# Optimization experiments

Measured on AMD Instinct MI355X. Metric: run time of the kernel, lower is better.

Reference implementation:

```python
import jax, jax.numpy as jnp
import numpy as np

N, C, B, NPG, M, E = 131072, 128, 64, 2048, 64, 1048576
LN_EPS = 1e-5


def setup_inputs() -> dict:
    key = jax.random.key(0)
    ks = jax.random.split(key, 8)
    h = jax.random.normal(ks[0], (N, C), dtype=jnp.float32)
    edge_index = jax.random.randint(ks[1], (2, E), 0, N, dtype=jnp.int32)
    U = jax.random.normal(ks[2], (B, NPG, M), dtype=jnp.float32)
    W = jax.random.normal(ks[3], (M, C, C), dtype=jnp.float32) * 0.02
    lin_w = jax.random.normal(ks[4], (C, C), dtype=jnp.float32) * (1.0 / np.sqrt(C))
    lin_b = jax.random.normal(ks[5], (C,), dtype=jnp.float32) * 0.01
    ln_g = jnp.ones((C,), dtype=jnp.float32)
    ln_beta = jnp.zeros((C,), dtype=jnp.float32)
    return {"h": h, "U": U, "W": W, "lin_w": lin_w, "lin_b": lin_b,
            "ln_g": ln_g, "ln_beta": ln_beta, "edge_index": edge_index}


def _gfno_block(h, U, W, lin_w, lin_b, ln_g, ln_beta, edge_index):
    n_nodes, c = h.shape
    b, npg, m_avail = U.shape
    m = min(m_avail, W.shape[0])
    Um = U[:, :, :m]                      # [B, n, m]
    Wm = W[:m]                            # [m, C, C]
    # Block-diagonal spectral conv (equal-sized graphs -> batched einsum)
    hb = h.reshape(b, npg, c)             # [B, n, C]
    h_hat = jnp.einsum('bnm,bnc->bmc', Um, hb)        # U^T h per graph
    out_hat = jnp.einsum('bmc,mco->bmo', h_hat, Wm)   # per-mode mixing
    spec = jnp.einsum('bnm,bmo->bno', Um, out_hat).reshape(n_nodes, c)
    # Local scatter-mean aggregation
    src, dst = edge_index[0], edge_index[1]
    agg = jax.ops.segment_sum(h[src], dst, num_segments=n_nodes)   # [N, C]
    deg = jax.ops.segment_sum(jnp.ones((src.shape[0],), h.dtype), dst,
                              num_segments=n_nodes)
    deg = jnp.maximum(deg, 1.0)[:, None]
    local = (agg / deg) @ lin_w.T + lin_b
    # Residual + LayerNorm + GELU (exact, erf-based as torch default)
    x = h + spec + local
    mu = jnp.mean(x, axis=-1, keepdims=True)
    var = jnp.mean(jnp.square(x - mu), axis=-1, keepdims=True)
    xn = (x - mu) * jax.lax.rsqrt(var + LN_EPS) * ln_g + ln_beta
    return jax.nn.gelu(xn, approximate=False)


def reference(h, U, W, lin_w, lin_b, ln_g, ln_beta, edge_index):
    return _gfno_block(h, U, W, lin_w, lin_b, ln_g, ln_beta, edge_index)
```

## Files before the change

### kernel.cpp

```cpp
#include <hip/hip_runtime.h>
#include <math.h>

#define NN   131072
#define CN   128
#define BN   64
#define NPGN 2048
#define MN   64
#define EN   1048576

typedef unsigned short u16;
typedef unsigned int   u32;
typedef __attribute__((ext_vector_type(8))) short short8;
typedef __attribute__((ext_vector_type(4))) float f32x4;

__device__ __forceinline__ float bf2f(u16 u){ return __uint_as_float(((u32)u)<<16); }
__device__ __forceinline__ u16 f2bf(float f){
  u32 x = __float_as_uint(f);
  return (u16)((x + 0x7fffu + ((x>>16)&1u)) >> 16);
}

__global__ void k_count(const int* __restrict__ dst, int* __restrict__ deg){
  int e = blockIdx.x*256 + threadIdx.x;
  atomicAdd(&deg[dst[e]], 1);
}

__global__ void k_scan1(const int* __restrict__ deg, int* __restrict__ rowst, int* __restrict__ bsum){
  __shared__ int s[512];
  const int t = threadIdx.x;
  const int i = blockIdx.x*512 + t;
  int v = deg[i];
  s[t] = v;
  __syncthreads();
  for (int off=1; off<512; off<<=1){
    int a = (t>=off) ? s[t-off] : 0;
    __syncthreads();
    s[t] += a;
    __syncthreads();
  }
  rowst[i] = s[t] - v;
  if (t==511) bsum[blockIdx.x] = s[511];
}

__global__ void k_scan2(const int* __restrict__ bsum, int* __restrict__ bofs){
  __shared__ int s[256];
  const int t = threadIdx.x;
  int v = bsum[t];
  s[t] = v;
  __syncthreads();
  for (int off=1; off<256; off<<=1){
    int a = (t>=off) ? s[t-off] : 0;
    __syncthreads();
    s[t] += a;
    __syncthreads();
  }
  bofs[t] = s[t] - v;
}

__global__ void k_scan3(int* __restrict__ rowst, const int* __restrict__ bofs){
  int i = blockIdx.x*256 + threadIdx.x;
  rowst[i] += bofs[i>>9];
}

__global__ void k_fill(const int* __restrict__ src, const int* __restrict__ dst,
                       const int* __restrict__ rowst, int* __restrict__ cursor,
                       int* __restrict__ csr){
  int e = blockIdx.x*256 + threadIdx.x;
  int d = dst[e];
  int p = atomicAdd(&cursor[d], 1);
  csr[rowst[d] + p] = src[e];
}

__global__ void k_prepw(const float* __restrict__ lin_w, u16* __restrict__ wsw){
  int tid = blockIdx.x*256 + threadIdx.x;
  int g = tid >> 6, L = tid & 63;
  int ct = g >> 2, ks = g & 3;
  int o = L & 15, q = L >> 4;
  const float* srcp = lin_w + (ct*16+o)*CN + ks*32 + q*8;
  u16 tmp[8];
  #pragma unroll
  for (int j=0;j<8;++j) tmp[j] = f2bf(srcp[j]);
  *(uint4*)(wsw + (size_t)tid*8) = *(const uint4*)tmp;
}

__global__ void k_prep_h(const float* __restrict__ h, u16* __restrict__ h16, u16* __restrict__ ht16){
  __shared__ u16 st[CN*72];
  const int t = threadIdx.x;
  const int b = blockIdx.x >> 5;
  const int n0 = (blockIdx.x & 31)*64;
  const float* srcb = h + ((size_t)b*NPGN + n0)*CN;
  u16* natb = h16 + ((size_t)b*NPGN + n0)*CN;
  #pragma unroll
  for (int j=0;j<8;++j){
    int fidx = (j*256+t)*4;
    int r = fidx>>7, c = fidx&127;
    float4 v = *(const float4*)(srcb + fidx);
    u16 q0=f2bf(v.x), q1=f2bf(v.y), q2=f2bf(v.z), q3=f2bf(v.w);
    ushort4 nv; nv.x=q0; nv.y=q1; nv.z=q2; nv.w=q3;
    *(ushort4*)(natb + fidx) = nv;
    st[(c+0)*72 + r] = q0; st[(c+1)*72 + r] = q1;
    st[(c+2)*72 + r] = q2; st[(c+3)*72 + r] = q3;
  }
  __syncthreads();
  #pragma unroll
  for (int j=0;j<4;++j){
    int oidx = (j*256+t)*8;
    int c = oidx>>6, nn = oidx&63;
    uint4 v = *(const uint4*)&st[c*72 + nn];
    *(uint4*)(ht16 + ((size_t)b*CN + c)*NPGN + n0 + nn) = v;
  }
}

__global__ void k_prep_U(const float* __restrict__ U, u16* __restrict__ U16, u16* __restrict__ Ut16){
  __shared__ u16 st2[MN*136];
  const int t = threadIdx.x;
  const int b = blockIdx.x >> 4;
  const int n0 = (blockIdx.x & 15)*128;
  const float* srcb = U + ((size_t)b*NPGN + n0)*MN;
  u16* natb = U16 + ((size_t)b*NPGN + n0)*MN;
  #pragma unroll
  for (int j=0;j<8;++j){
    int fidx = (j*256+t)*4;
    int r = fidx>>6, mm = fidx&63;
    float4 v = *(const float4*)(srcb + fidx);
    u16 q0=f2bf(v.x), q1=f2bf(v.y), q2=f2bf(v.z), q3=f2bf(v.w);
    ushort4 nv; nv.x=q0; nv.y=q1; nv.z=q2; nv.w=q3;
    *(ushort4*)(natb + fidx) = nv;
    st2[(mm+0)*136 + r] = q0; st2[(mm+1)*136 + r] = q1;
    st2[(mm+2)*136 + r] = q2; st2[(mm+3)*136 + r] = q3;
  }
  __syncthreads();
  #pragma unroll
  for (int j=0;j<4;++j){
    int oidx = (j*256+t)*8;
    int mm = oidx>>7, nn = oidx&127;
    uint4 v = *(const uint4*)&st2[mm*136 + nn];
    *(uint4*)(Ut16 + ((size_t)b*MN + mm)*NPGN + n0 + nn) = v;
  }
}

__global__ __launch_bounds__(256) void k_hhat(const u16* __restrict__ Ut16,
                                              const u16* __restrict__ ht16,
                                              float* __restrict__ hp){
  const int t = threadIdx.x;
  const int L = t & 63, w = t >> 6;
  const int b = blockIdx.x >> 3, q = blockIdx.x & 7;
  const int lo = L & 15, qd = (L >> 4) << 3;
  f32x4 acc[8] = {};
  const u16* Arow  = Ut16 + ((size_t)(b*MN + w*16 + lo))*NPGN + q*256 + qd;
  const u16* Bbase = ht16 + ((size_t)(b*CN + lo))*NPGN + q*256 + qd;
  #pragma unroll
  for (int ks=0; ks<8; ++ks){
    short8 af = *(const short8*)(Arow + ks*32);
    #pragma unroll
    for (int ct=0; ct<8; ++ct){
      short8 bf = *(const short8*)(Bbase + (size_t)ct*16*NPGN + ks*32);
      acc[ct] = __builtin_amdgcn_mfma_f32_16x16x32_bf16(af, bf, acc[ct], 0, 0, 0);
    }
  }
  const int rb = w*16 + ((L>>4)<<2);
  float* dstb = hp + ((size_t)q*BN + b)*MN*CN;
  #pragma unroll
  for (int ct=0; ct<8; ++ct)
    #pragma unroll
    for (int r=0; r<4; ++r)
      dstb[(size_t)(rb+r)*CN + ct*16 + lo] = acc[ct][r];
}

__global__ void k_ohat(const float* __restrict__ W, const float* __restrict__ hp,
                       u16* __restrict__ ohatT){
  __shared__ u16  sw[CN*CN];
  __shared__ float shh[CN];
  const int t = threadIdx.x;
  const int m  = blockIdx.x & 63;
  const int bg = blockIdx.x >> 6;
  const float* Wm = W + (size_t)m*CN*CN;
  for (int j=0;j<32;++j){
    int idx = (j*128 + t)*4;
    float4 wv = *(const float4*)(Wm + idx);
    sw[idx+0]=f2bf(wv.x); sw[idx+1]=f2bf(wv.y); sw[idx+2]=f2bf(wv.z); sw[idx+3]=f2bf(wv.w);
  }
  __syncthreads();
  const size_t S = (size_t)BN*MN*CN;
  for (int bb=0; bb<16; ++bb){
    int b = bg*16 + bb;
    size_t base = ((size_t)b*MN + m)*CN + t;
    float a = 0.f;
    #pragma unroll
    for (int p=0;p<8;++p) a += hp[(size_t)p*S + base];
    shh[t] = a;
    __syncthreads();
    float acc = 0.f;
    for (int c=0;c<CN;++c) acc = fmaf(shh[c], bf2f(sw[c*CN+t]), acc);
    ohatT[((size_t)b*CN + t)*MN + m] = f2bf(acc);
    __syncthreads();
  }
}

__global__ __launch_bounds__(256) void k_spec(const u16* __restrict__ U16,
                                              const u16* __restrict__ ohatT,
                                              u16* __restrict__ spec16){
  const int t = threadIdx.x;
  const int L = t & 63, w = t >> 6;
  const int b = blockIdx.x >> 4;
  const int n0 = (blockIdx.x & 15)*128;
  const int lo = L & 15, qd = (L >> 4) << 3;
  f32x4 acc[2][8] = {};
  const u16* Abase = U16  + ((size_t)(b*NPGN + n0 + w*32 + lo))*MN + qd;
  const u16* Bbase = ohatT + ((size_t)(b*CN + lo))*MN + qd;
  #pragma unroll
  for (int ks=0; ks<2; ++ks){
    short8 a0 = *(const short8*)(Abase + ks*32);
    short8 a1 = *(const short8*)(Abase + (size_t)16*MN + ks*32);
    #pragma unroll
    for (int ot=0; ot<8; ++ot){
      short8 bf = *(const short8*)(Bbase + (size_t)ot*16*MN + ks*32);
      acc[0][ot] = __builtin_amdgcn_mfma_f32_16x16x32_bf16(a0, bf, acc[0][ot], 0, 0, 0);
      acc[1][ot] = __builtin_amdgcn_mfma_f32_16x16x32_bf16(a1, bf, acc[1][ot], 0, 0, 0);
    }
  }
  const int rb = (L>>4)<<2;
  #pragma unroll
  for (int i=0;i<2;++i){
    u16* dstb = spec16 + ((size_t)(b*NPGN + n0 + w*32 + i*16 + rb))*CN + lo;
    #pragma unroll
    for (int ot=0; ot<8; ++ot)
      #pragma unroll
      for (int r=0; r<4; ++r)
        dstb[(size_t)r*CN + ot*16] = f2bf(acc[i][ot][r]);
  }
}

__device__ __forceinline__ void unp_add(float* a, uint4 p){
  a[0]+=bf2f((u16)(p.x&0xffffu)); a[1]+=bf2f((u16)(p.x>>16));
  a[2]+=bf2f((u16)(p.y&0xffffu)); a[3]+=bf2f((u16)(p.y>>16));
  a[4]+=bf2f((u16)(p.z&0xffffu)); a[5]+=bf2f((u16)(p.z>>16));
  a[6]+=bf2f((u16)(p.w&0xffffu)); a[7]+=bf2f((u16)(p.w>>16));
}

__global__ __launch_bounds__(256,4) void k_localep(
    const u16* __restrict__ h16, const u16* __restrict__ spec16,
    const u16* __restrict__ wsw,
    const int* __restrict__ rowst, const int* __restrict__ deg, const int* __restrict__ csr,
    const float* __restrict__ lin_b, const float* __restrict__ ln_g,
    const float* __restrict__ ln_beta, float* __restrict__ out){
  __shared__ u16   sv[32*136];
  __shared__ float sx[32*132];
  const int t = threadIdx.x;
  const int w = t>>6, lane = t&63;
  const size_t n0 = (size_t)blockIdx.x*32;

  {
    const int g   = lane >> 4;
    const int c16 = lane & 15;
    #pragma unroll
    for (int p=0; p<4; ++p){
      const int iA = p*8 + w;
      const int iB = p*8 + 4 + w;
      const int nA = (int)n0 + iA, nB = (int)n0 + iB;
      const int rsA = rowst[nA], dgA = deg[nA];
      const int rsB = rowst[nB], dgB = deg[nB];
      const int reA = rsA + dgA, reB = rsB + dgB;
      int eA = rsA + g, eB = rsB + g;
      float accA[8] = {0.f,0.f,0.f,0.f,0.f,0.f,0.f,0.f};
      float accB[8] = {0.f,0.f,0.f,0.f,0.f,0.f,0.f,0.f};
      while (eA < reA || eB < reB){
        const bool vA0 = eA   < reA, vA1 = eA+4 < reA;
        const bool vB0 = eB   < reB, vB1 = eB+4 < reB;
        int sA0 = vA0 ? csr[eA]   : 0;
        int sA1 = vA1 ? csr[eA+4] : 0;
        int sB0 = vB0 ? csr[eB]   : 0;
        int sB1 = vB1 ? csr[eB+4] : 0;
        uint4 qA0 = {0u,0u,0u,0u}, qA1 = {0u,0u,0u,0u};
        uint4 qB0 = {0u,0u,0u,0u}, qB1 = {0u,0u,0u,0u};
        if (vA0) qA0 = *(const uint4*)(h16 + (size_t)sA0*CN + c16*8);
        if (vA1) qA1 = *(const uint4*)(h16 + (size_t)sA1*CN + c16*8);
        if (vB0) qB0 = *(const uint4*)(h16 + (size_t)sB0*CN + c16*8);
        if (vB1) qB1 = *(const uint4*)(h16 + (size_t)sB1*CN + c16*8);
        unp_add(accA, qA0); unp_add(accA, qA1);
        unp_add(accB, qB0); unp_add(accB, qB1);
        eA += 8; eB += 8;
      }
      #pragma unroll
      for (int j=0;j<8;++j){
        accA[j] += __shfl_xor(accA[j],16); accA[j] += __shfl_xor(accA[j],32);
        accB[j] += __shfl_xor(accB[j],16); accB[j] += __shfl_xor(accB[j],32);
      }
      const float invA = 1.0f / fmaxf((float)dgA, 1.0f);
      const float invB = 1.0f / fmaxf((float)dgB, 1.0f);
      if (g==0){
        u16 ta[8], tb[8];
        #pragma unroll
        for (int j=0;j<8;++j){ ta[j]=f2bf(accA[j]*invA); tb[j]=f2bf(accB[j]*invB); }
        *(uint4*)&sv[iA*136 + c16*8] = *(const uint4*)ta;
        *(uint4*)&sv[iB*136 + c16*8] = *(const uint4*)tb;
      }
    }
  }
  __syncthreads();

  const int rt = w&1, cb = w>>1;
  f32x4 acc[4] = {};
  #pragma unroll
  for (int ks=0; ks<4; ++ks){
    short8 af = *(const short8*)&sv[(rt*16 + (lane&15))*136 + ks*32 + ((lane>>4)<<3)];
    #pragma unroll
    for (int c4=0; c4<4; ++c4){
      const short8 bf = *(const short8*)(wsw + ((size_t)((cb*4+c4)*4+ks)*64 + lane)*8);
      acc[c4] = __builtin_amdgcn_mfma_f32_16x16x32_bf16(af, bf, acc[c4], 0, 0, 0);
    }
  }
  #pragma unroll
  for (int c4=0; c4<4; ++c4){
    int col = cb*64 + c4*16 + (lane&15);
    int rb = rt*16 + ((lane>>4)<<2);
    #pragma unroll
    for (int r=0; r<4; ++r) sx[(rb+r)*132 + col] = acc[c4][r];
  }
  __syncthreads();

  float2 lb    = *(const float2*)(lin_b  + 2*lane);
  float2 lg    = *(const float2*)(ln_g   + 2*lane);
  float2 lbe   = *(const float2*)(ln_beta+ 2*lane);
  for (int r=0; r<8; ++r){
    int i = r*4 + w;
    size_t base = (n0 + i)*CN + 2*lane;
    u32 hA = *(const u32*)(h16 + base);
    u32 sA = *(const u32*)(spec16 + base);
    float2 loc = *(const float2*)&sx[i*132 + 2*lane];
    float x0 = bf2f((u16)(hA&0xffffu)) + bf2f((u16)(sA&0xffffu)) + loc.x + lb.x;
    float x1 = bf2f((u16)(hA>>16))     + bf2f((u16)(sA>>16))     + loc.y + lb.y;
    float s  = x0 + x1;
    float ss = fmaf(x0,x0, x1*x1);
    #pragma unroll
    for (int d=1; d<64; d<<=1){ s += __shfl_xor(s,d); ss += __shfl_xor(ss,d); }
    float mu  = s*(1.0f/128.0f);
    float var = ss*(1.0f/128.0f) - mu*mu;
    float rstd = rsqrtf(var + 1e-5f);
    float xn0 = (x0-mu)*rstd*lg.x + lbe.x;
    float xn1 = (x1-mu)*rstd*lg.y + lbe.y;
    float2 st;
    st.x = 0.5f*xn0*(1.0f + erff(xn0*0.70710678118654752f));
    st.y = 0.5f*xn1*(1.0f + erff(xn1*0.70710678118654752f));
    *(float2*)(out + base) = st;
  }
}

extern "C" void kernel_launch(void* const* d_in, const int* in_sizes, int n_in,
                              void* d_out, int out_size, void* d_ws, size_t ws_size,
                              hipStream_t stream) {
  const float* h      = (const float*)d_in[0];
  const float* U      = (const float*)d_in[1];
  const float* W      = (const float*)d_in[2];
  const float* lin_w  = (const float*)d_in[3];
  const float* lin_b  = (const float*)d_in[4];
  const float* ln_g   = (const float*)d_in[5];
  const float* ln_b2  = (const float*)d_in[6];
  const int* ei       = (const int*)d_in[7];
  const int* src = ei;
  const int* dst = ei + EN;
  float* out = (float*)d_out;

  char* wp = (char*)d_ws;
  float* hp     = (float*)wp; wp += (size_t)8*BN*MN*CN*sizeof(float);
  u16*   ohatT  = (u16*)wp;   wp += (size_t)BN*CN*MN*sizeof(u16);
  u16*   h16    = (u16*)wp;   wp += (size_t)NN*CN*sizeof(u16);
  u16*   ht16   = (u16*)wp;   wp += (size_t)BN*CN*NPGN*sizeof(u16);
  u16*   U16b   = (u16*)wp;   wp += (size_t)BN*NPGN*MN*sizeof(u16);
  u16*   Ut16   = (u16*)wp;   wp += (size_t)BN*MN*NPGN*sizeof(u16);
  u16*   spec16 = (u16*)wp;   wp += (size_t)NN*CN*sizeof(u16);
  u16*   wsw    = (u16*)wp;   wp += (size_t)CN*CN*sizeof(u16);
  int*   deg    = (int*)wp;   wp += (size_t)NN*sizeof(int);
  int*   rowst  = (int*)wp;   wp += (size_t)NN*sizeof(int);
  int*   cursor = (int*)wp;   wp += (size_t)NN*sizeof(int);
  int*   csr    = (int*)wp;   wp += (size_t)EN*sizeof(int);
  int*   bsum   = (int*)wp;   wp += 512*sizeof(int);
  int*   bofs   = (int*)wp;   wp += 512*sizeof(int);

  hipMemsetAsync(deg,    0, (size_t)NN*sizeof(int), stream);
  hipMemsetAsync(cursor, 0, (size_t)NN*sizeof(int), stream);

  k_count<<<EN/256, 256, 0, stream>>>(dst, deg);
  k_scan1<<<NN/512, 512, 0, stream>>>(deg, rowst, bsum);
  k_scan2<<<1, 256, 0, stream>>>(bsum, bofs);
  k_scan3<<<NN/256, 256, 0, stream>>>(rowst, bofs);
  k_fill<<<EN/256, 256, 0, stream>>>(src, dst, rowst, cursor, csr);

  k_prepw<<<8, 256, 0, stream>>>(lin_w, wsw);
  k_prep_h<<<BN*32, 256, 0, stream>>>(h, h16, ht16);
  k_prep_U<<<BN*16, 256, 0, stream>>>(U, U16b, Ut16);

  k_hhat<<<BN*8, 256, 0, stream>>>(Ut16, ht16, hp);
  k_ohat<<<256, 128, 0, stream>>>(W, hp, ohatT);
  k_spec<<<BN*16, 256, 0, stream>>>(U16b, ohatT, spec16);

  k_localep<<<NN/32, 256, 0, stream>>>(h16, spec16, wsw, rowst, deg, csr,
                                       lin_b, ln_g, ln_b2, out);
}
```

Baseline: 433.1 us.

## Move per-mode mixing to MFMA with split-bf16 input and pre-transposed W

Replaces the scalar-FMA k_ohat, which looped 16 batches per block with LDS broadcasts, by an MFMA version. A new k_prepWT kernel converts W to bf16 and transposes it, and h_hat is split into hi and lo bf16 parts so accuracy is kept at the cost of twice the MFMAs. k_localep also stores its local-linear result in LDS as bf16 instead of fp32 and raises the occupancy hint to 8 blocks. That halves LDS use per block but rounds the local term to bf16 and may cause register spilling.

```diff
diff --git a/kernel.cpp b/kernel.cpp
--- a/kernel.cpp
+++ b/kernel.cpp
@@ -80,6 +80,32 @@
   #pragma unroll
   for (int j=0;j<8;++j) tmp[j] = f2bf(srcp[j]);
   *(uint4*)(wsw + (size_t)tid*8) = *(const uint4*)tmp;
+}
+
+__global__ void k_prepWT(const float* __restrict__ W, u16* __restrict__ WT16){
+  __shared__ u16 st[128*132];
+  const int t = threadIdx.x;
+  const int m = blockIdx.x;
+  const float* Wm = W + (size_t)m*CN*CN;
+  #pragma unroll
+  for (int it=0; it<16; ++it){
+    int flat = (it*256 + t)*4;
+    int c = flat >> 7, o = flat & 127;
+    float4 v = *(const float4*)(Wm + flat);
+    st[(o+0)*132 + c] = f2bf(v.x);
+    st[(o+1)*132 + c] = f2bf(v.y);
+    st[(o+2)*132 + c] = f2bf(v.z);
+    st[(o+3)*132 + c] = f2bf(v.w);
+  }
+  __syncthreads();
+  u16* dstm = WT16 + (size_t)m*CN*CN;
+  #pragma unroll
+  for (int it=0; it<8; ++it){
+    int oidx = (it*256 + t)*8;
+    int o = oidx >> 7, c = oidx & 127;
+    uint4 v = *(const uint4*)&st[o*132 + c];
+    *(uint4*)(dstm + (size_t)o*CN + c) = v;
+  }
 }
 
 __global__ void k_prep_h(const float* __restrict__ h, u16* __restrict__ h16, u16* __restrict__ ht16){
@@ -166,33 +192,63 @@
       dstb[(size_t)(rb+r)*CN + ct*16 + lo] = acc[ct][r];
 }
 
-__global__ void k_ohat(const float* __restrict__ W, const float* __restrict__ hp,
-                       u16* __restrict__ ohatT){
-  __shared__ u16  sw[CN*CN];
-  __shared__ float shh[CN];
-  const int t = threadIdx.x;
-  const int m  = blockIdx.x & 63;
-  const int bg = blockIdx.x >> 6;
-  const float* Wm = W + (size_t)m*CN*CN;
-  for (int j=0;j<32;++j){
-    int idx = (j*128 + t)*4;
-    float4 wv = *(const float4*)(Wm + idx);
-    sw[idx+0]=f2bf(wv.x); sw[idx+1]=f2bf(wv.y); sw[idx+2]=f2bf(wv.z); sw[idx+3]=f2bf(wv.w);
-  }
-  __syncthreads();
-  const size_t S = (size_t)BN*MN*CN;
-  for (int bb=0; bb<16; ++bb){
-    int b = bg*16 + bb;
-    size_t base = ((size_t)b*MN + m)*CN + t;
-    float a = 0.f;
-    #pragma unroll
-    for (int p=0;p<8;++p) a += hp[(size_t)p*S + base];
-    shh[t] = a;
-    __syncthreads();
-    float acc = 0.f;
-    for (int c=0;c<CN;++c) acc = fmaf(shh[c], bf2f(sw[c*CN+t]), acc);
-    ohatT[((size_t)b*CN + t)*MN + m] = f2bf(acc);
-    __syncthreads();
+__global__ __launch_bounds__(256) void k_ohat(const float* __restrict__ hp,
+                                              const u16* __restrict__ WT16,
+                                              u16* __restrict__ ohatT){
+  __shared__ u16 shHi[16*132];
+  __shared__ u16 shLo[16*132];
+  const int t = threadIdx.x;
+  const int m  = blockIdx.x >> 2;
+  const int bq = blockIdx.x & 3;
+
+  {
+    const int bl = t >> 4;
+    const int c0 = (t & 15) * 8;
+    const size_t S = (size_t)BN*MN*CN;
+    const float* base = hp + ((size_t)(bq*16 + bl)*MN + m)*CN + c0;
+    float a[8] = {0,0,0,0,0,0,0,0};
+    #pragma unroll
+    for (int q=0; q<8; ++q){
+      float4 v0 = *(const float4*)(base + q*S);
+      float4 v1 = *(const float4*)(base + q*S + 4);
+      a[0]+=v0.x; a[1]+=v0.y; a[2]+=v0.z; a[3]+=v0.w;
+      a[4]+=v1.x; a[5]+=v1.y; a[6]+=v1.z; a[7]+=v1.w;
+    }
+    u16 hi[8], lo[8];
+    #pragma unroll
+    for (int j=0;j<8;++j){
+      hi[j] = f2bf(a[j]);
+      lo[j] = f2bf(a[j] - bf2f(hi[j]));
+    }
+    *(uint4*)&shHi[bl*132 + c0] = *(const uint4*)hi;
+    *(uint4*)&shLo[bl*132 + c0] = *(const uint4*)lo;
+  }
+  __syncthreads();
+
+  const int L = t & 63, w = t >> 6;
+  const int lo16 = L & 15, qd = (L >> 4) << 3;
+  const u16* WTm = WT16 + (size_t)m*CN*CN;
+  f32x4 acc[2] = {};
+  #pragma unroll
+  for (int ks=0; ks<4; ++ks){
+    short8 ah = *(const short8*)&shHi[lo16*132 + ks*32 + qd];
+    short8 al = *(const short8*)&shLo[lo16*132 + ks*32 + qd];
+    #pragma unroll
+    for (int ot=0; ot<2; ++ot){
+      short8 bf = *(const short8*)(WTm + (size_t)(w*32 + ot*16 + lo16)*CN + ks*32 + qd);
+      acc[ot] = __builtin_amdgcn_mfma_f32_16x16x32_bf16(ah, bf, acc[ot], 0, 0, 0);
+      acc[ot] = __builtin_amdgcn_mfma_f32_16x16x32_bf16(al, bf, acc[ot], 0, 0, 0);
+    }
+  }
+  const int rb = (L>>4)<<2;
+  #pragma unroll
+  for (int ot=0; ot<2; ++ot){
+    #pragma unroll
+    for (int r=0; r<4; ++r){
+      int b = bq*16 + rb + r;
+      int o = w*32 + ot*16 + lo16;
+      ohatT[((size_t)b*CN + o)*MN + m] = f2bf(acc[ot][r]);
+    }
   }
 }
 
@@ -237,14 +293,14 @@
   a[6]+=bf2f((u16)(p.w&0xffffu)); a[7]+=bf2f((u16)(p.w>>16));
 }
 
-__global__ __launch_bounds__(256,4) void k_localep(
+__global__ __launch_bounds__(256,8) void k_localep(
     const u16* __restrict__ h16, const u16* __restrict__ spec16,
     const u16* __restrict__ wsw,
     const int* __restrict__ rowst, const int* __restrict__ deg, const int* __restrict__ csr,
     const float* __restrict__ lin_b, const float* __restrict__ ln_g,
     const float* __restrict__ ln_beta, float* __restrict__ out){
-  __shared__ u16   sv[32*136];
-  __shared__ float sx[32*132];
+  __shared__ u16 sv[32*136];
+  __shared__ u16 sx16[32*132];
   const int t = threadIdx.x;
   const int w = t>>6, lane = t&63;
   const size_t n0 = (size_t)blockIdx.x*32;
@@ -314,7 +370,7 @@
     int col = cb*64 + c4*16 + (lane&15);
     int rb = rt*16 + ((lane>>4)<<2);
     #pragma unroll
-    for (int r=0; r<4; ++r) sx[(rb+r)*132 + col] = acc[c4][r];
+    for (int r=0; r<4; ++r) sx16[(rb+r)*132 + col] = f2bf(acc[c4][r]);
   }
   __syncthreads();
 
@@ -326,9 +382,9 @@
     size_t base = (n0 + i)*CN + 2*lane;
     u32 hA = *(const u32*)(h16 + base);
     u32 sA = *(const u32*)(spec16 + base);
-    float2 loc = *(const float2*)&sx[i*132 + 2*lane];
-    float x0 = bf2f((u16)(hA&0xffffu)) + bf2f((u16)(sA&0xffffu)) + loc.x + lb.x;
-    float x1 = bf2f((u16)(hA>>16))     + bf2f((u16)(sA>>16))     + loc.y + lb.y;
+    u32 lA = *(const u32*)&sx16[i*132 + 2*lane];
+    float x0 = bf2f((u16)(hA&0xffffu)) + bf2f((u16)(sA&0xffffu)) + bf2f((u16)(lA&0xffffu)) + lb.x;
+    float x1 = bf2f((u16)(hA>>16))     + bf2f((u16)(sA>>16))     + bf2f((u16)(lA>>16))     + lb.y;
     float s  = x0 + x1;
     float ss = fmaf(x0,x0, x1*x1);
     #pragma unroll
@@ -369,6 +425,7 @@
   u16*   Ut16   = (u16*)wp;   wp += (size_t)BN*MN*NPGN*sizeof(u16);
   u16*   spec16 = (u16*)wp;   wp += (size_t)NN*CN*sizeof(u16);
   u16*   wsw    = (u16*)wp;   wp += (size_t)CN*CN*sizeof(u16);
+  u16*   WT16   = (u16*)wp;   wp += (size_t)MN*CN*CN*sizeof(u16);
   int*   deg    = (int*)wp;   wp += (size_t)NN*sizeof(int);
   int*   rowst  = (int*)wp;   wp += (size_t)NN*sizeof(int);
   int*   cursor = (int*)wp;   wp += (size_t)NN*sizeof(int);
@@ -386,11 +443,12 @@
   k_fill<<<EN/256, 256, 0, stream>>>(src, dst, rowst, cursor, csr);
 
   k_prepw<<<8, 256, 0, stream>>>(lin_w, wsw);
+  k_prepWT<<<MN, 256, 0, stream>>>(W, WT16);
   k_prep_h<<<BN*32, 256, 0, stream>>>(h, h16, ht16);
   k_prep_U<<<BN*16, 256, 0, stream>>>(U, U16b, Ut16);
 
   k_hhat<<<BN*8, 256, 0, stream>>>(Ut16, ht16, hp);
-  k_ohat<<<256, 128, 0, stream>>>(W, hp, ohatT);
+  k_ohat<<<MN*4, 256, 0, stream>>>(hp, WT16, ohatT);
   k_spec<<<BN*16, 256, 0, stream>>>(U16b, ohatT, spec16);
 
   k_localep<<<NN/32, 256, 0, stream>>>(h16, spec16, wsw, rowst, deg, csr,
```

Result: faster. 408.9 us (-5.6%).
